# Optimization experiments

Hardware: AMD Instinct MI355X
Metric: run time of the kernel (lower is better)

The kernel has to match this reference:

```python
import jax, jax.numpy as jnp
import numpy as np

N_NODES = 100000
N_EDGES = 3200000


def gcn_conv(x, src, dst, W, b, n_nodes):
    # PyG GCNConv with default add_self_loops=True, symmetric normalization.
    # src/dst already include self-loops. deg computed on destination.
    ones = jnp.ones(src.shape[0], dtype=x.dtype)
    deg = jax.ops.segment_sum(ones, dst, num_segments=n_nodes)
    dinv = jnp.where(deg > 0, jax.lax.rsqrt(deg), 0.0).astype(x.dtype)
    norm = dinv[src] * dinv[dst]                      # [E]
    h = x @ W                                         # linear first (PyG order)
    msg = h[src] * norm[:, None]                      # gather + scale
    out = jax.ops.segment_sum(msg, dst, num_segments=n_nodes)  # scatter-add
    return out + b


def setup_inputs() -> dict:
    key = jax.random.key(0)
    k1, k2, k3, k4 = jax.random.split(key, 4)
    x = jax.random.normal(k1, (N_NODES, 4), dtype=jnp.float32)
    edge_index = jax.random.randint(k2, (2, N_EDGES), 0, N_NODES, dtype=jnp.int64)
    W1 = jax.random.normal(k3, (4, 32), dtype=jnp.float32) * 0.5
    b1 = jnp.zeros((32,), dtype=jnp.float32)
    W2 = jax.random.normal(k4, (32, 1), dtype=jnp.float32) * 0.2
    b2 = jnp.zeros((1,), dtype=jnp.float32)
    return {"x": x, "edge_index": edge_index, "W1": W1, "b1": b1, "W2": W2, "b2": b2}


def reference(x, edge_index, W1, b1, W2, b2):
    n = x.shape[0]
    # add self-loops once; same augmented graph used by both convs
    loops = jnp.arange(n, dtype=edge_index.dtype)
    src = jnp.concatenate([edge_index[0], loops])
    dst = jnp.concatenate([edge_index[1], loops])
    h = jax.nn.relu(gcn_conv(x, src, dst, W1, b1, n))
    out = jax.nn.sigmoid(gcn_conv(h, src, dst, W2, b2, n))
    return out.squeeze(-1)  # [N] anomaly probability
```

## Files before the change

### kernel.cpp

```cpp
#include <hip/hip_runtime.h>
#include <math.h>
#include <stdint.h>


#define BINBITS 8
#define BINSZ   256
#define NBMAX   512
#define EBC     256
#define THR     256
#define QS      2097152.0f
#define SENT    0xFFFFFFFFu

__device__ __forceinline__ uint32_t packq(float v) {
    return __float2uint_rn(fmaf(v, QS, 16.0f * QS));
}


__global__ void countK(const int* __restrict__ dst, uint32_t* __restrict__ bc,
                       int e, int nb) {
    __shared__ uint32_t cnt[NBMAX];
    int t = threadIdx.x, b = blockIdx.x;
    for (int i = t; i < nb; i += THR) cnt[i] = 0;
    __syncthreads();
    int epb = (e + EBC - 1) / EBC;
    int lo = b * epb, hi = min(e, lo + epb);
    if (((lo | hi) & 3) == 0 && (((uintptr_t)dst & 15) == 0)) {
        const int4* dst4 = (const int4*)dst;
        for (int i = lo / 4 + t; i < hi / 4; i += THR) {
            int4 v = dst4[i];
            atomicAdd(&cnt[((unsigned)v.x) >> BINBITS], 1u);
            atomicAdd(&cnt[((unsigned)v.y) >> BINBITS], 1u);
            atomicAdd(&cnt[((unsigned)v.z) >> BINBITS], 1u);
            atomicAdd(&cnt[((unsigned)v.w) >> BINBITS], 1u);
        }
    } else {
        for (int i = lo + t; i < hi; i += THR)
            atomicAdd(&cnt[((unsigned)dst[i]) >> BINBITS], 1u);
    }
    __syncthreads();
    for (int i = t; i < nb; i += THR) bc[(size_t)i * EBC + b] = cnt[i];
}

__global__ void scan1K(uint32_t* __restrict__ bc, uint32_t* __restrict__ binSum) {
    __shared__ uint32_t s[EBC];
    int t = threadIdx.x, bin = blockIdx.x;
    uint32_t v = bc[(size_t)bin * EBC + t];
    s[t] = v;
    __syncthreads();
    for (int off = 1; off < EBC; off <<= 1) {
        uint32_t u = (t >= off) ? s[t - off] : 0u;
        __syncthreads();
        s[t] += u;
        __syncthreads();
    }
    bc[(size_t)bin * EBC + t] = s[t] - v;
    if (t == EBC - 1) binSum[bin] = s[t];
}

__global__ void scan2K(const uint32_t* __restrict__ binSum,
                       uint32_t* __restrict__ binStart,
                       uint32_t* __restrict__ records, int nb) {
    __shared__ uint32_t s[512];
    int t = threadIdx.x;
    uint32_t real = (t < nb) ? binSum[t] : 0u;
    uint32_t v = (real + 3u) & ~3u;
    s[t] = v;
    __syncthreads();
    for (int off = 1; off < 512; off <<= 1) {
        uint32_t u = (t >= off) ? s[t - off] : 0u;
        __syncthreads();
        s[t] += u;
        __syncthreads();
    }
    if (t < nb) {
        uint32_t start = s[t] - v;
        binStart[t] = start;
        for (uint32_t q = start + real; q < start + v; ++q) records[q] = SENT;
    }
    if (t == nb - 1) binStart[nb] = s[t];
}

__global__ void fillK(const int* __restrict__ src, const int* __restrict__ dst,
                      const uint32_t* __restrict__ bc,
                      const uint32_t* __restrict__ binStart,
                      uint32_t* __restrict__ records, int e, int nb) {
    __shared__ uint32_t cur[NBMAX];
    int t = threadIdx.x;
    int b = (blockIdx.x & 7) * (EBC / 8) + (blockIdx.x >> 3);
    for (int i = t; i < nb; i += THR)
        cur[i] = bc[(size_t)i * EBC + b] + binStart[i];
    __syncthreads();
    int epb = (e + EBC - 1) / EBC;
    int lo = b * epb, hi = min(e, lo + epb);
    if (((lo | hi) & 3) == 0 && (((uintptr_t)src & 15) == 0) && (((uintptr_t)dst & 15) == 0)) {
        const int4* src4 = (const int4*)src;
        const int4* dst4 = (const int4*)dst;
        for (int i = lo / 4 + t; i < hi / 4; i += THR) {
            int4 dv = dst4[i];
            int4 sv = src4[i];
            unsigned d0 = (unsigned)dv.x, d1 = (unsigned)dv.y;
            unsigned d2 = (unsigned)dv.z, d3 = (unsigned)dv.w;
            uint32_t p0 = atomicAdd(&cur[d0 >> BINBITS], 1u);
            records[p0] = (((unsigned)sv.x) << BINBITS) | (d0 & (BINSZ - 1));
            uint32_t p1 = atomicAdd(&cur[d1 >> BINBITS], 1u);
            records[p1] = (((unsigned)sv.y) << BINBITS) | (d1 & (BINSZ - 1));
            uint32_t p2 = atomicAdd(&cur[d2 >> BINBITS], 1u);
            records[p2] = (((unsigned)sv.z) << BINBITS) | (d2 & (BINSZ - 1));
            uint32_t p3 = atomicAdd(&cur[d3 >> BINBITS], 1u);
            records[p3] = (((unsigned)sv.w) << BINBITS) | (d3 & (BINSZ - 1));
        }
    } else {
        for (int i = lo + t; i < hi; i += THR) {
            unsigned d = (unsigned)dst[i];
            unsigned s = (unsigned)src[i];
            uint32_t slot = atomicAdd(&cur[d >> BINBITS], 1u);
            records[slot] = (s << BINBITS) | (d & (BINSZ - 1));
        }
    }
}


__global__ void deg_part(const uint32_t* __restrict__ records,
                         const uint32_t* __restrict__ binStart,
                         uint32_t* __restrict__ histP, int split) {
    __shared__ uint32_t hist[BINSZ];
    int t = threadIdx.x;
    int bin = blockIdx.x / split, sub = blockIdx.x % split;
    hist[t] = 0u;
    __syncthreads();
    uint32_t lo = binStart[bin], hi = binStart[bin + 1];
    uint32_t chunk = (((hi - lo + split - 1) / split) + 3u) & ~3u;
    uint32_t slo = lo + sub * chunk;
    uint32_t shi = min(hi, slo + chunk);
    const uint4* rec4 = (const uint4*)records;
    for (uint32_t i = slo / 4 + t; i < shi / 4; i += THR) {
        uint4 r = rec4[i];
        if (r.x != SENT) atomicAdd(&hist[r.x & (BINSZ - 1)], 1u);
        if (r.y != SENT) atomicAdd(&hist[r.y & (BINSZ - 1)], 1u);
        if (r.z != SENT) atomicAdd(&hist[r.z & (BINSZ - 1)], 1u);
        if (r.w != SENT) atomicAdd(&hist[r.w & (BINSZ - 1)], 1u);
    }
    __syncthreads();
    histP[(size_t)blockIdx.x * BINSZ + t] = hist[t];
}

__global__ void mergeDinvY(const uint32_t* __restrict__ histP,
                           const float4* __restrict__ x4,
                           float* __restrict__ dinv, uint32_t* __restrict__ deg,
                           ulonglong2* __restrict__ y4q, int split, int n) {
    int t = threadIdx.x, bin = blockIdx.x;
    int node = (bin << BINBITS) + t;
    if (node >= n) return;
    uint32_t c = 0;
    for (int s = 0; s < split; ++s)
        c += histP[(size_t)(bin * split + s) * BINSZ + t];
    float dd = rsqrtf(1.0f + (float)c);
    dinv[node] = dd;
    deg[node] = c;
    float4 xv = x4[node];
    uint32_t q0 = packq(dd * xv.x), q1 = packq(dd * xv.y);
    uint32_t q2 = packq(dd * xv.z), q3 = packq(dd * xv.w);
    ulonglong2 p;
    p.x = ((unsigned long long)q1 << 32) | q0;
    p.y = ((unsigned long long)q3 << 32) | q2;
    y4q[node] = p;
}


__global__ void agg_part(const uint32_t* __restrict__ records,
                         const uint32_t* __restrict__ binStart,
                         const ulonglong2* __restrict__ y4q,
                         unsigned long long* __restrict__ aggP, int split) {
    __shared__ unsigned long long acc[2 * BINSZ];
    int t = threadIdx.x;
    int bin = blockIdx.x / split, sub = blockIdx.x % split;
    acc[t] = 0ull;
    acc[BINSZ + t] = 0ull;
    __syncthreads();
    uint32_t lo = binStart[bin], hi = binStart[bin + 1];
    uint32_t chunk = (((hi - lo + split - 1) / split) + 3u) & ~3u;
    uint32_t slo = lo + sub * chunk;
    uint32_t shi = min(hi, slo + chunk);
    const uint4* rec4 = (const uint4*)records;
    for (uint32_t i = slo / 4 + t; i < shi / 4; i += THR) {
        uint4 r = rec4[i];
        unsigned s0 = (r.x == SENT) ? 0u : (r.x >> BINBITS);
        unsigned s1 = (r.y == SENT) ? 0u : (r.y >> BINBITS);
        unsigned s2 = (r.z == SENT) ? 0u : (r.z >> BINBITS);
        unsigned s3 = (r.w == SENT) ? 0u : (r.w >> BINBITS);
        ulonglong2 y0 = y4q[s0];
        ulonglong2 y1 = y4q[s1];
        ulonglong2 y2 = y4q[s2];
        ulonglong2 y3 = y4q[s3];
        if (r.x != SENT) { unsigned d = r.x & (BINSZ - 1); atomicAdd(&acc[d], y0.x); atomicAdd(&acc[BINSZ + d], y0.y); }
        if (r.y != SENT) { unsigned d = r.y & (BINSZ - 1); atomicAdd(&acc[d], y1.x); atomicAdd(&acc[BINSZ + d], y1.y); }
        if (r.z != SENT) { unsigned d = r.z & (BINSZ - 1); atomicAdd(&acc[d], y2.x); atomicAdd(&acc[BINSZ + d], y2.y); }
        if (r.w != SENT) { unsigned d = r.w & (BINSZ - 1); atomicAdd(&acc[d], y3.x); atomicAdd(&acc[BINSZ + d], y3.y); }
    }
    __syncthreads();
    unsigned long long* p = aggP + (size_t)blockIdx.x * (2 * BINSZ);
    p[t] = acc[t];
    p[BINSZ + t] = acc[BINSZ + t];
}

__global__ void mergeAggT(const unsigned long long* __restrict__ aggP,
                          const float* __restrict__ dinv, const uint32_t* __restrict__ deg,
                          const float4* __restrict__ x4,
                          const float* __restrict__ W1, const float* __restrict__ b1,
                          const float* __restrict__ W2,
                          float* __restrict__ g, int split, int n) {
    __shared__ float sW1[128], sb1[32], sW2[32];
    int t = threadIdx.x, bin = blockIdx.x;
    if (t < 128) sW1[t] = W1[t];
    else if (t < 160) sb1[t - 128] = b1[t - 128];
    else if (t < 192) sW2[t - 160] = W2[t - 160];
    __syncthreads();
    int node = (bin << BINBITS) + t;
    if (node >= n) return;
    unsigned long long s0lo = 0, s0hi = 0, s1lo = 0, s1hi = 0;
    size_t base = (size_t)bin * split * (2 * BINSZ);
    for (int s2 = 0; s2 < split; ++s2) {
        const unsigned long long* q = aggP + base + (size_t)s2 * (2 * BINSZ);
        unsigned long long P0 = q[t], P1 = q[BINSZ + t];
        s0lo += (uint32_t)P0; s0hi += (uint32_t)(P0 >> 32);
        s1lo += (uint32_t)P1; s1hi += (uint32_t)(P1 >> 32);
    }
    long long bias = (long long)deg[node] << 25;
    const float inv = 1.0f / QS;
    long long v0 = (long long)s0lo - bias, v1 = (long long)s0hi - bias;
    long long v2 = (long long)s1lo - bias, v3 = (long long)s1hi - bias;
    float T0 = (float)(v0 >> 21) + (float)(v0 & 0x1FFFFF) * inv;
    float T1 = (float)(v1 >> 21) + (float)(v1 & 0x1FFFFF) * inv;
    float T2 = (float)(v2 >> 21) + (float)(v2 & 0x1FFFFF) * inv;
    float T3 = (float)(v3 >> 21) + (float)(v3 & 0x1FFFFF) * inv;
    float dd = dinv[node];
    float4 xv = x4[node];
    float a0 = dd * (T0 + dd * xv.x), a1 = dd * (T1 + dd * xv.y);
    float a2 = dd * (T2 + dd * xv.z), a3 = dd * (T3 + dd * xv.w);
    float hv = 0.f;
#pragma unroll
    for (int j = 0; j < 32; ++j) {
        float o = fmaf(a0, sW1[j], fmaf(a1, sW1[32 + j],
                  fmaf(a2, sW1[64 + j], fmaf(a3, sW1[96 + j], sb1[j]))));
        hv += fmaxf(o, 0.f) * sW2[j];
    }
    g[node] = dd * hv;
}


__global__ void out_part(const uint32_t* __restrict__ records,
                         const uint32_t* __restrict__ binStart,
                         const float* __restrict__ g,
                         float* __restrict__ outP, int split) {
    __shared__ float accg[BINSZ];
    int t = threadIdx.x;
    int bin = blockIdx.x / split, sub = blockIdx.x % split;
    accg[t] = 0.f;
    __syncthreads();
    uint32_t lo = binStart[bin], hi = binStart[bin + 1];
    uint32_t chunk = (((hi - lo + split - 1) / split) + 3u) & ~3u;
    uint32_t slo = lo + sub * chunk;
    uint32_t shi = min(hi, slo + chunk);
    const uint4* rec4 = (const uint4*)records;
    for (uint32_t i = slo / 4 + t; i < shi / 4; i += THR) {
        uint4 r = rec4[i];
        unsigned s0 = (r.x == SENT) ? 0u : (r.x >> BINBITS);
        unsigned s1 = (r.y == SENT) ? 0u : (r.y >> BINBITS);
        unsigned s2 = (r.z == SENT) ? 0u : (r.z >> BINBITS);
        unsigned s3 = (r.w == SENT) ? 0u : (r.w >> BINBITS);
        float g0 = g[s0], g1 = g[s1], g2 = g[s2], g3 = g[s3];
        if (r.x != SENT) atomicAdd(&accg[r.x & (BINSZ - 1)], g0);
        if (r.y != SENT) atomicAdd(&accg[r.y & (BINSZ - 1)], g1);
        if (r.z != SENT) atomicAdd(&accg[r.z & (BINSZ - 1)], g2);
        if (r.w != SENT) atomicAdd(&accg[r.w & (BINSZ - 1)], g3);
    }
    __syncthreads();
    outP[(size_t)blockIdx.x * BINSZ + t] = accg[t];
}

__global__ void mergeOutK(const float* __restrict__ outP, const float* __restrict__ g,
                          const float* __restrict__ dinv, const float* __restrict__ b2,
                          float* __restrict__ out, int split, int n) {
    int t = threadIdx.x, bin = blockIdx.x;
    int node = (bin << BINBITS) + t;
    if (node >= n) return;
    float s = 0.f;
    size_t base = (size_t)bin * split * BINSZ;
    for (int k = 0; k < split; ++k)
        s += outP[base + (size_t)k * BINSZ + t];
    float v = dinv[node] * (s + g[node]) + b2[0];
    out[node] = 1.0f / (1.0f + expf(-v));
}


extern "C" void kernel_launch(void* const* d_in, const int* in_sizes, int n_in,
                              void* d_out, int out_size, void* d_ws, size_t ws_size,
                              hipStream_t stream) {
    const float* x  = (const float*)d_in[0];
    const int*   ei = (const int*)d_in[1];
    const float* W1 = (const float*)d_in[2];
    const float* b1 = (const float*)d_in[3];
    const float* W2 = (const float*)d_in[4];
    const float* b2 = (const float*)d_in[5];
    float* out = (float*)d_out;

    const int n = in_sizes[0] / 4;
    const int e = in_sizes[1] / 2;
    const int* src = ei;
    const int* dst = ei + e;

    const int nb = (n + BINSZ - 1) >> BINBITS;

    size_t recB  = (((size_t)e + 4 * (size_t)nb) * 4 + 15) & ~(size_t)15;
    size_t bcB   = ((size_t)nb * EBC * 4 + 15) & ~(size_t)15;
    size_t bsB   = ((size_t)(2 * nb + 2) * 4 + 15) & ~(size_t)15;
    size_t dinvB = ((size_t)n * 4 + 15) & ~(size_t)15;
    size_t degB  = ((size_t)n * 4 + 15) & ~(size_t)15;
    size_t gB    = ((size_t)n * 4 + 15) & ~(size_t)15;
    size_t y4qB  = ((size_t)n * 16 + 15) & ~(size_t)15;
    size_t fixed = recB + bcB + bsB + dinvB + degB + gB + y4qB;

    auto arena_sz = [&](int s) { return (size_t)nb * s * (2 * BINSZ) * 8; };

    int split;
    if      (ws_size >= fixed + arena_sz(16)) split = 16;
    else if (ws_size >= fixed + arena_sz(8))  split = 8;
    else if (ws_size >= fixed + arena_sz(4))  split = 4;
    else if (ws_size >= fixed + arena_sz(2))  split = 2;
    else                                      split = 1;

    char* p = (char*)d_ws;
    uint32_t*   records  = (uint32_t*)p;      p += recB;
    uint32_t*   bc       = (uint32_t*)p;      p += bcB;
    uint32_t*   binStart = (uint32_t*)p;      p += bsB;
    uint32_t*   binSum   = binStart + nb + 1;
    float*      dinv     = (float*)p;         p += dinvB;
    uint32_t*   deg      = (uint32_t*)p;      p += degB;
    float*      gbuf     = (float*)p;         p += gB;
    ulonglong2* y4q      = (ulonglong2*)p;    p += y4qB;
    void*       arena    = (void*)p;

    const float4* x4 = (const float4*)x;

    countK<<<EBC, THR, 0, stream>>>(dst, bc, e, nb);
    scan1K<<<nb, EBC, 0, stream>>>(bc, binSum);
    scan2K<<<1, 512, 0, stream>>>(binSum, binStart, records, nb);
    fillK <<<EBC, THR, 0, stream>>>(src, dst, bc, binStart, records, e, nb);

    deg_part<<<nb * split, THR, 0, stream>>>(records, binStart, (uint32_t*)arena, split);
    mergeDinvY<<<nb, THR, 0, stream>>>((const uint32_t*)arena, x4, dinv, deg, y4q, split, n);
    agg_part<<<nb * split, THR, 0, stream>>>(records, binStart, y4q,
                                             (unsigned long long*)arena, split);
    mergeAggT<<<nb, THR, 0, stream>>>((const unsigned long long*)arena, dinv, deg, x4,
                                      W1, b1, W2, gbuf, split, n);
    out_part<<<nb * split, THR, 0, stream>>>(records, binStart, gbuf, (float*)arena, split);
    mergeOutK<<<nb, THR, 0, stream>>>((const float*)arena, gbuf, dinv, b2, out, split, n);
}
```

Before: 102.5 us.

## Fuse degree and output split-reduce passes into single 1024-thread per-bin kernels

```diff
diff --git a/kernel.cpp b/kernel.cpp
--- a/kernel.cpp
+++ b/kernel.cpp
@@ -120,20 +120,19 @@
 }
 
 
-__global__ void deg_part(const uint32_t* __restrict__ records,
-                         const uint32_t* __restrict__ binStart,
-                         uint32_t* __restrict__ histP, int split) {
+__global__ __launch_bounds__(1024)
+void degInline(const uint32_t* __restrict__ records,
+               const uint32_t* __restrict__ binStart,
+               const float4* __restrict__ x4,
+               float* __restrict__ dinv, uint32_t* __restrict__ deg,
+               ulonglong2* __restrict__ y4q, int n) {
     __shared__ uint32_t hist[BINSZ];
-    int t = threadIdx.x;
-    int bin = blockIdx.x / split, sub = blockIdx.x % split;
-    hist[t] = 0u;
+    int t = threadIdx.x, bin = blockIdx.x;
+    if (t < BINSZ) hist[t] = 0u;
     __syncthreads();
     uint32_t lo = binStart[bin], hi = binStart[bin + 1];
-    uint32_t chunk = (((hi - lo + split - 1) / split) + 3u) & ~3u;
-    uint32_t slo = lo + sub * chunk;
-    uint32_t shi = min(hi, slo + chunk);
     const uint4* rec4 = (const uint4*)records;
-    for (uint32_t i = slo / 4 + t; i < shi / 4; i += THR) {
+    for (uint32_t i = lo / 4 + t; i < hi / 4; i += 1024) {
         uint4 r = rec4[i];
         if (r.x != SENT) atomicAdd(&hist[r.x & (BINSZ - 1)], 1u);
         if (r.y != SENT) atomicAdd(&hist[r.y & (BINSZ - 1)], 1u);
@@ -141,19 +140,10 @@
         if (r.w != SENT) atomicAdd(&hist[r.w & (BINSZ - 1)], 1u);
     }
     __syncthreads();
-    histP[(size_t)blockIdx.x * BINSZ + t] = hist[t];
-}
-
-__global__ void mergeDinvY(const uint32_t* __restrict__ histP,
-                           const float4* __restrict__ x4,
-                           float* __restrict__ dinv, uint32_t* __restrict__ deg,
-                           ulonglong2* __restrict__ y4q, int split, int n) {
-    int t = threadIdx.x, bin = blockIdx.x;
+    if (t >= BINSZ) return;
     int node = (bin << BINBITS) + t;
     if (node >= n) return;
-    uint32_t c = 0;
-    for (int s = 0; s < split; ++s)
-        c += histP[(size_t)(bin * split + s) * BINSZ + t];
+    uint32_t c = hist[t];
     float dd = rsqrtf(1.0f + (float)c);
     dinv[node] = dd;
     deg[node] = c;
@@ -248,21 +238,18 @@
 }
 
 
-__global__ void out_part(const uint32_t* __restrict__ records,
-                         const uint32_t* __restrict__ binStart,
-                         const float* __restrict__ g,
-                         float* __restrict__ outP, int split) {
+__global__ __launch_bounds__(1024)
+void outInline(const uint32_t* __restrict__ records,
+               const uint32_t* __restrict__ binStart,
+               const float* __restrict__ g, const float* __restrict__ dinv,
+               const float* __restrict__ b2, float* __restrict__ out, int n) {
     __shared__ float accg[BINSZ];
-    int t = threadIdx.x;
-    int bin = blockIdx.x / split, sub = blockIdx.x % split;
-    accg[t] = 0.f;
+    int t = threadIdx.x, bin = blockIdx.x;
+    if (t < BINSZ) accg[t] = 0.f;
     __syncthreads();
     uint32_t lo = binStart[bin], hi = binStart[bin + 1];
-    uint32_t chunk = (((hi - lo + split - 1) / split) + 3u) & ~3u;
-    uint32_t slo = lo + sub * chunk;
-    uint32_t shi = min(hi, slo + chunk);
     const uint4* rec4 = (const uint4*)records;
-    for (uint32_t i = slo / 4 + t; i < shi / 4; i += THR) {
+    for (uint32_t i = lo / 4 + t; i < hi / 4; i += 1024) {
         uint4 r = rec4[i];
         unsigned s0 = (r.x == SENT) ? 0u : (r.x >> BINBITS);
         unsigned s1 = (r.y == SENT) ? 0u : (r.y >> BINBITS);
@@ -275,20 +262,10 @@
         if (r.w != SENT) atomicAdd(&accg[r.w & (BINSZ - 1)], g3);
     }
     __syncthreads();
-    outP[(size_t)blockIdx.x * BINSZ + t] = accg[t];
-}
-
-__global__ void mergeOutK(const float* __restrict__ outP, const float* __restrict__ g,
-                          const float* __restrict__ dinv, const float* __restrict__ b2,
-                          float* __restrict__ out, int split, int n) {
-    int t = threadIdx.x, bin = blockIdx.x;
+    if (t >= BINSZ) return;
     int node = (bin << BINBITS) + t;
     if (node >= n) return;
-    float s = 0.f;
-    size_t base = (size_t)bin * split * BINSZ;
-    for (int k = 0; k < split; ++k)
-        s += outP[base + (size_t)k * BINSZ + t];
-    float v = dinv[node] * (s + g[node]) + b2[0];
+    float v = dinv[node] * (accg[t] + g[node]) + b2[0];
     out[node] = 1.0f / (1.0f + expf(-v));
 }
 
@@ -323,11 +300,10 @@
     auto arena_sz = [&](int s) { return (size_t)nb * s * (2 * BINSZ) * 8; };
 
     int split;
-    if      (ws_size >= fixed + arena_sz(16)) split = 16;
-    else if (ws_size >= fixed + arena_sz(8))  split = 8;
-    else if (ws_size >= fixed + arena_sz(4))  split = 4;
-    else if (ws_size >= fixed + arena_sz(2))  split = 2;
-    else                                      split = 1;
+    if      (ws_size >= fixed + arena_sz(8)) split = 8;
+    else if (ws_size >= fixed + arena_sz(4)) split = 4;
+    else if (ws_size >= fixed + arena_sz(2)) split = 2;
+    else                                     split = 1;
 
     char* p = (char*)d_ws;
     uint32_t*   records  = (uint32_t*)p;      p += recB;
@@ -347,12 +323,10 @@
     scan2K<<<1, 512, 0, stream>>>(binSum, binStart, records, nb);
     fillK <<<EBC, THR, 0, stream>>>(src, dst, bc, binStart, records, e, nb);
 
-    deg_part<<<nb * split, THR, 0, stream>>>(records, binStart, (uint32_t*)arena, split);
-    mergeDinvY<<<nb, THR, 0, stream>>>((const uint32_t*)arena, x4, dinv, deg, y4q, split, n);
+    degInline<<<nb, 1024, 0, stream>>>(records, binStart, x4, dinv, deg, y4q, n);
     agg_part<<<nb * split, THR, 0, stream>>>(records, binStart, y4q,
                                              (unsigned long long*)arena, split);
     mergeAggT<<<nb, THR, 0, stream>>>((const unsigned long long*)arena, dinv, deg, x4,
                                       W1, b1, W2, gbuf, split, n);
-    out_part<<<nb * split, THR, 0, stream>>>(records, binStart, gbuf, (float*)arena, split);
-    mergeOutK<<<nb, THR, 0, stream>>>((const float*)arena, gbuf, dinv, b2, out, split, n);
-}
+    outInline<<<nb, 1024, 0, stream>>>(records, binStart, gbuf, dinv, b2, out, n);
+}
```

Result: faster. 90.32 us (-11.9%).
